# Kernel optimization log

Hardware: AMD Instinct MI355X
Metric: run time of the kernel (lower is better)

Reference implementation:

```python
import jax, jax.numpy as jnp
import numpy as np

NUM_BINS_X = 128; NUM_BINS_Y = 128
XL, XH, YL, YH = 0.0, 1000.0, 0.0, 1000.0
NUM_NETS = 100000
NUM_NODES = 200000
NUM_MOVABLE = 180000
NUM_PINS = 400000
UNIT_H_CAP = 1.5
UNIT_V_CAP = 1.4
MAX_RATE = 2.0
MIN_RATE = 1.0 / MAX_RATE
BIN_SX = (XH - XL) / NUM_BINS_X
BIN_SY = (YH - YL) / NUM_BINS_Y


def setup_inputs() -> dict:
    key = jax.random.key(0)
    k1, k2, k3, k4, k5, k6, k7, k8 = jax.random.split(key, 8)
    pos = jnp.concatenate([
        jax.random.uniform(k1, (NUM_NODES,), jnp.float32, XL, XH - 8.0),
        jax.random.uniform(k2, (NUM_NODES,), jnp.float32, YL, YH - 8.0)])
    pin_pos = jnp.concatenate([
        jax.random.uniform(k3, (NUM_PINS,), jnp.float32, XL, XH),
        jax.random.uniform(k4, (NUM_PINS,), jnp.float32, YL, YH)])
    node_size_x = jax.random.uniform(k5, (NUM_NODES,), jnp.float32, 1.0, 8.0)
    node_size_y = jax.random.uniform(k6, (NUM_NODES,), jnp.float32, 1.0, 8.0)
    # 4 pins per net (uniform ragged layout); flat_netpin is a permutation of pins
    netpin_start = jnp.arange(NUM_NETS + 1, dtype=jnp.int32) * (NUM_PINS // NUM_NETS)
    flat_netpin = jax.random.permutation(k7, NUM_PINS).astype(jnp.int32)
    net_weights = jax.random.uniform(k8, (NUM_NETS,), jnp.float32, 0.5, 1.5)
    return dict(pos=pos, pin_pos=pin_pos, node_size_x=node_size_x,
                node_size_y=node_size_y, net_weights=net_weights,
                netpin_start=netpin_start, flat_netpin=flat_netpin)


def _bin_edges(lo, size, n):
    l = lo + jnp.arange(n, dtype=jnp.float32) * size
    return l, l + size


def _overlap(lo_e, hi_e, lo, hi):
    # per-interval overlap of [lo, hi] with each bin [lo_e, hi_e]; >=0
    return jnp.clip(jnp.minimum(hi_e[None, :], hi[:, None]) -
                    jnp.maximum(lo_e[None, :], lo[:, None]), 0.0, None)


def reference(pos, pin_pos, node_size_x, node_size_y, net_weights,
              netpin_start, flat_netpin):
    # ---- phase 1: per-net bbox (ragged gather) + RUDY demand binning ----
    lengths = netpin_start[1:] - netpin_start[:-1]                      # [N]
    net_ids = jnp.repeat(jnp.arange(NUM_NETS, dtype=jnp.int32), lengths,
                         total_repeat_length=NUM_PINS)                  # [P]
    px = pin_pos[flat_netpin]
    py = pin_pos[flat_netpin + NUM_PINS]
    x_min = jax.ops.segment_min(px, net_ids, num_segments=NUM_NETS)
    x_max = jax.ops.segment_max(px, net_ids, num_segments=NUM_NETS)
    y_min = jax.ops.segment_min(py, net_ids, num_segments=NUM_NETS)
    y_max = jax.ops.segment_max(py, net_ids, num_segments=NUM_NETS)

    bxl, bxr = _bin_edges(XL, BIN_SX, NUM_BINS_X)
    byl, byr = _bin_edges(YL, BIN_SY, NUM_BINS_Y)
    ox = _overlap(bxl, bxr, x_min, x_max)                               # [N, BX]
    oy = _overlap(byl, byr, y_min, y_max)                               # [N, BY]
    dx = x_max - x_min
    dy = y_max - y_min
    # horizontal demand per bin = wt * overlap / (y_max - y_min); vertical analog
    cx = jnp.where(dy > 0, net_weights / jnp.where(dy > 0, dy, 1.0), 0.0)
    cy = jnp.where(dx > 0, net_weights / jnp.where(dx > 0, dx, 1.0), 0.0)
    map_x = jnp.einsum('nx,ny->xy', ox * cx[:, None], oy)               # [BX, BY]
    map_y = jnp.einsum('nx,ny->xy', ox * cy[:, None], oy)

    bin_area = BIN_SX * BIN_SY
    ux = map_x / (bin_area * UNIT_H_CAP)
    uy = map_y / (bin_area * UNIT_V_CAP)
    util = jnp.clip(jnp.maximum(ux, uy), MIN_RATE, MAX_RATE)            # [BX, BY]

    # ---- phase 2: per movable node, overlap-weighted utilization read-back ----
    nx = pos[:NUM_MOVABLE]
    ny = pos[NUM_NODES:NUM_NODES + NUM_MOVABLE]
    sx = node_size_x[:NUM_MOVABLE]
    sy = node_size_y[:NUM_MOVABLE]
    oxn = _overlap(bxl, bxr, nx, nx + sx)                               # [M, BX]
    oyn = _overlap(byl, byr, ny, ny + sy)                               # [M, BY]
    tmp = jnp.einsum('mx,xy->my', oxn, util)                            # [M, BY]
    instance_route_area = jnp.sum(tmp * oyn, axis=1)                    # [M]
    return instance_route_area
```

## Files before the change

### kernel.cpp

```cpp
#include <hip/hip_runtime.h>

constexpr int   NB         = 128;
constexpr int   NCELL      = NB * NB;
constexpr float S          = 7.8125f;
constexpr int   NUM_NETS   = 100000;
constexpr int   NUM_NODES  = 200000;
constexpr int   NUM_MOVABLE= 180000;
constexpr int   NUM_PINS   = 400000;
constexpr float UNIT_H_CAP = 1.5f;
constexpr float UNIT_V_CAP = 1.4f;

#define TPB    512
#define NDB    256
#define NCHUNK 4

__device__ __forceinline__ float edgef(int t) { return (float)t * S; }

__device__ __forceinline__ int bin_of(float v) {
    int t = (int)floorf(v / S);
    while (edgef(t + 1) <= v) ++t;
    while (edgef(t)     >  v) --t;
    return t;
}

__device__ __forceinline__ float phi(int t, float lo, float hi) {
    return fminf(fmaxf(edgef(t), lo), hi);
}

__device__ __forceinline__ int second_diff(float lo, float hi,
                                           int* idx, float* val) {
    int a = bin_of(lo);
    int b = bin_of(hi);
    int n = 0;
    idx[n] = a;
    val[n] = phi(a + 1, lo, hi) - 2.f * phi(a, lo, hi) + phi(a - 1, lo, hi);
    ++n;
    idx[n] = a + 1;
    val[n] = phi(a + 2, lo, hi) - 2.f * phi(a + 1, lo, hi) + phi(a, lo, hi);
    ++n;
    if (b > a + 1) {
        idx[n] = b;
        val[n] = phi(b + 1, lo, hi) - 2.f * phi(b, lo, hi) + phi(b - 1, lo, hi);
        ++n;
    }
    if (b > a) {
        idx[n] = b + 1;
        val[n] = phi(b + 2, lo, hi) - 2.f * phi(b + 1, lo, hi) + phi(b, lo, hi);
        ++n;
    }
    return n;
}

__global__ __launch_bounds__(TPB) void net_diff_kernel(
    const float* __restrict__ pin_pos,
    const float* __restrict__ net_weights,
    const int*   __restrict__ nps,
    const int*   __restrict__ fnp,
    float* __restrict__ Px, float* __restrict__ Py) {
    __shared__ float D[NCELL];
    const int tid = threadIdx.x;
    const int n   = blockIdx.x * TPB + tid;
    const bool have = (n < NUM_NETS);

    float4* D4 = (float4*)D;
    for (int i = tid; i < NCELL / 4; i += TPB) D4[i] = make_float4(0,0,0,0);

    float cx = 0.f, cy = 0.f;
    int ixs[4], iys[4];
    float vxs[4], vys[4];
    int nx = 0, ny = 0;

    if (have) {
        int s = nps[n], e = nps[n + 1];
        float xmin = 1e30f, xmax = -1e30f, ymin = 1e30f, ymax = -1e30f;
        if (e - s == 4 && (s & 3) == 0) {
            int4 p4 = *(const int4*)(fnp + s);
            float x0 = pin_pos[p4.x], y0 = pin_pos[p4.x + NUM_PINS];
            float x1 = pin_pos[p4.y], y1 = pin_pos[p4.y + NUM_PINS];
            float x2 = pin_pos[p4.z], y2 = pin_pos[p4.z + NUM_PINS];
            float x3 = pin_pos[p4.w], y3 = pin_pos[p4.w + NUM_PINS];
            xmin = fminf(fminf(x0, x1), fminf(x2, x3));
            xmax = fmaxf(fmaxf(x0, x1), fmaxf(x2, x3));
            ymin = fminf(fminf(y0, y1), fminf(y2, y3));
            ymax = fmaxf(fmaxf(y0, y1), fmaxf(y2, y3));
        } else {
            for (int p = s; p < e; ++p) {
                int pin = fnp[p];
                float px = pin_pos[pin];
                float py = pin_pos[pin + NUM_PINS];
                xmin = fminf(xmin, px); xmax = fmaxf(xmax, px);
                ymin = fminf(ymin, py); ymax = fmaxf(ymax, py);
            }
        }
        if (e > s) {
            float w  = net_weights[n];
            float dx = xmax - xmin, dy = ymax - ymin;
            cx = (dy > 0.f) ? w / dy : 0.f;
            cy = (dx > 0.f) ? w / dx : 0.f;
            if (cx != 0.f || cy != 0.f) {
                nx = second_diff(xmin, xmax, ixs, vxs);
                ny = second_diff(ymin, ymax, iys, vys);
            }
        }
    }
    __syncthreads();

    if (have && cx != 0.f) {
        for (int i = 0; i < nx; ++i) {
            int row = ixs[i];
            float cfi = cx * vxs[i];
            if (cfi == 0.f || row >= NB) continue;
            for (int j = 0; j < ny; ++j) {
                int col = iys[j];
                float t = cfi * vys[j];
                if (t == 0.f || col >= NB) continue;
                atomicAdd(&D[row * NB + col], t);
            }
        }
    }
    __syncthreads();
    {
        float4* P = (float4*)(Px + (size_t)blockIdx.x * NCELL);
        for (int i = tid; i < NCELL / 4; i += TPB) {
            P[i] = D4[i];
            D4[i] = make_float4(0,0,0,0);
        }
    }
    __syncthreads();

    if (have && cy != 0.f) {
        for (int i = 0; i < nx; ++i) {
            int row = ixs[i];
            float cfi = cy * vxs[i];
            if (cfi == 0.f || row >= NB) continue;
            for (int j = 0; j < ny; ++j) {
                int col = iys[j];
                float t = cfi * vys[j];
                if (t == 0.f || col >= NB) continue;
                atomicAdd(&D[row * NB + col], t);
            }
        }
    }
    __syncthreads();
    {
        float4* P = (float4*)(Py + (size_t)blockIdx.x * NCELL);
        for (int i = tid; i < NCELL / 4; i += TPB) P[i] = D4[i];
    }
}

__global__ __launch_bounds__(256) void reduce_kernel(
    const float4* __restrict__ Px, const float4* __restrict__ Py,
    float4* __restrict__ R, int B) {
    constexpr int NC4 = NCELL / 4;
    int t = blockIdx.x * blockDim.x + threadIdx.x;
    int chunk = blockIdx.y;
    if (t >= 2 * NC4) return;
    int m  = (t < NC4) ? 0 : 1;
    int c4 = t & (NC4 - 1);
    const float4* P = m ? Py : Px;
    int per = (B + NCHUNK - 1) / NCHUNK;
    int b0 = chunk * per;
    int b1 = min(b0 + per, B);
    float4 a0 = {0,0,0,0}, a1 = {0,0,0,0};
    int b = b0;
    for (; b + 1 < b1; b += 2) {
        float4 v0 = P[(size_t)b * NC4 + c4];
        float4 v1 = P[(size_t)(b + 1) * NC4 + c4];
        a0.x += v0.x; a0.y += v0.y; a0.z += v0.z; a0.w += v0.w;
        a1.x += v1.x; a1.y += v1.y; a1.z += v1.z; a1.w += v1.w;
    }
    for (; b < b1; ++b) {
        float4 v = P[(size_t)b * NC4 + c4];
        a0.x += v.x; a0.y += v.y; a0.z += v.z; a0.w += v.w;
    }
    float4 r;
    r.x = a0.x + a1.x; r.y = a0.y + a1.y; r.z = a0.z + a1.z; r.w = a0.w + a1.w;
    R[((size_t)(chunk * 2 + m)) * NC4 + c4] = r;
}

__global__ __launch_bounds__(256) void finish_kernel(
    const float* __restrict__ R,
    float* __restrict__ Xp,
    float* __restrict__ util) {
    int t = threadIdx.x;
    int m   = (t >= NB) ? 1 : 0;
    int col = t & (NB - 1);
    const float* Ra = R + (size_t)m * NCELL;
    float* O = Xp + (size_t)m * NCELL;
    float acc = 0.f;
    #pragma unroll 8
    for (int i = 0; i < NB; ++i) {
        int idx = i * NB + col;
        float v = Ra[idx] + Ra[2 * NCELL + idx] + Ra[4 * NCELL + idx]
                + Ra[6 * NCELL + idx];
        acc += v;
        O[idx] = acc;
    }
    __syncthreads();
    if (t < NB) {
        constexpr float invx = 1.f / (S * S * UNIT_H_CAP);
        constexpr float invy = 1.f / (S * S * UNIT_V_CAP);
        const float* Xx = Xp;
        const float* Xy = Xp + NCELL;
        float ax = 0.f, ay = 0.f;
        #pragma unroll 8
        for (int j = 0; j < NB; ++j) {
            int idx = t * NB + j;
            ax += Xx[idx];
            ay += Xy[idx];
            float u = fmaxf(ax * invx, ay * invy);
            util[idx] = fminf(fmaxf(u, 0.5f), 2.0f);
        }
    }
}

__global__ __launch_bounds__(256) void node_kernel(
    const float* __restrict__ pos,
    const float* __restrict__ nsx,
    const float* __restrict__ nsy,
    const float* __restrict__ util,
    float* __restrict__ out) {
    int m = blockIdx.x * blockDim.x + threadIdx.x;
    if (m >= NUM_MOVABLE) return;
    float x  = pos[m];
    float y  = pos[NUM_NODES + m];
    float xh = x + nsx[m];
    float yh = y + nsy[m];
    int ax = max(0,      (int)floorf(x  / S) - 1);
    int bx = min(NB - 1, (int)floorf(xh / S) + 1);
    int ay = max(0,      (int)floorf(y  / S) - 1);
    int by = min(NB - 1, (int)floorf(yh / S) + 1);
    float acc = 0.f;
    for (int i = ax; i <= bx; ++i) {
        float ov = fminf(edgef(i + 1), xh) - fmaxf(edgef(i), x);
        if (ov <= 0.f) continue;
        float inner = 0.f;
        for (int j = ay; j <= by; ++j) {
            float ovy = fminf(edgef(j + 1), yh) - fmaxf(edgef(j), y);
            if (ovy > 0.f) inner += ovy * util[i * NB + j];
        }
        acc += ov * inner;
    }
    out[m] = acc;
}

extern "C" void kernel_launch(void* const* d_in, const int* in_sizes, int n_in,
                              void* d_out, int out_size, void* d_ws, size_t ws_size,
                              hipStream_t stream) {
    const float* pos      = (const float*)d_in[0];
    const float* pin_pos  = (const float*)d_in[1];
    const float* nsx      = (const float*)d_in[2];
    const float* nsy      = (const float*)d_in[3];
    const float* nw       = (const float*)d_in[4];
    const int*   npstart  = (const int*)d_in[5];
    const int*   fnp      = (const int*)d_in[6];
    float*       out      = (float*)d_out;

    float* w    = (float*)d_ws;
    float* R    = w;                       w += NCHUNK * 2 * NCELL;
    float* Xp   = w;                       w += 2 * NCELL;
    float* util = w;                       w += NCELL;
    float* Px   = w;

    size_t fixed = (size_t)(w - (float*)d_ws) * sizeof(float);
    int B = NDB;
    if (ws_size > fixed) {
        size_t fit = (ws_size - fixed) / ((size_t)2 * NCELL * sizeof(float));
        if ((size_t)B > fit) B = (int)fit;
    } else {
        B = 1;
    }
    if (B < 1) B = 1;
    float* Py = Px + (size_t)B * NCELL;

    net_diff_kernel<<<B, TPB, 0, stream>>>(pin_pos, nw, npstart, fnp, Px, Py);
    {
        dim3 g((2 * (NCELL / 4) + 255) / 256, NCHUNK);
        reduce_kernel<<<g, 256, 0, stream>>>(
            (const float4*)Px, (const float4*)Py, (float4*)R, B);
    }
    finish_kernel<<<1, 256, 0, stream>>>(R, Xp, util);
    node_kernel<<<(NUM_MOVABLE + 255) / 256, 256, 0, stream>>>(
        pos, nsx, nsy, util, out);
}
```

Baseline: 133.1 us.

## Interleave partial-sum reduction across 8 slices and prefetch pin loads before smem clear

The reduce kernel now splits the per-block partial maps into 8 interleaved slices (block index strided by NPAR) instead of 4 contiguous chunks, and uses 4 accumulators per thread for more memory-level parallelism. The finish kernel sums 8 partials instead of 4. In the net kernel, pin-position and weight gathers are issued before the shared-memory zeroing loop so their latency overlaps the clear. The risks are more partial-result traffic and more serial summation work in the single-block finish kernel, and the launch hardcodes 256 reduce blocks, which assumes 2*NC4/256 = 32 slices times 8.

New measurement: 142.1 us. 6.8% more time.

```diff
diff --git a/kernel.cpp b/kernel.cpp
--- a/kernel.cpp
+++ b/kernel.cpp
@@ -12,7 +12,7 @@
 
 #define TPB    512
 #define NDB    256
-#define NCHUNK 4
+#define NPAR   8
 
 __device__ __forceinline__ float edgef(int t) { return (float)t * S; }
 
@@ -62,6 +62,22 @@
     const int n   = blockIdx.x * TPB + tid;
     const bool have = (n < NUM_NETS);
 
+    float x0=0,x1=0,x2=0,x3=0,y0=0,y1=0,y2=0,y3=0,w=0;
+    int s = 0, e = 0;
+    bool fast = false;
+    if (have) {
+        s = nps[n]; e = nps[n + 1];
+        fast = (e - s == 4) && ((s & 3) == 0);
+        if (fast) {
+            int4 p4 = *(const int4*)(fnp + s);
+            x0 = pin_pos[p4.x]; y0 = pin_pos[p4.x + NUM_PINS];
+            x1 = pin_pos[p4.y]; y1 = pin_pos[p4.y + NUM_PINS];
+            x2 = pin_pos[p4.z]; y2 = pin_pos[p4.z + NUM_PINS];
+            x3 = pin_pos[p4.w]; y3 = pin_pos[p4.w + NUM_PINS];
+            w  = net_weights[n];
+        }
+    }
+
     float4* D4 = (float4*)D;
     for (int i = tid; i < NCELL / 4; i += TPB) D4[i] = make_float4(0,0,0,0);
 
@@ -71,19 +87,14 @@
     int nx = 0, ny = 0;
 
     if (have) {
-        int s = nps[n], e = nps[n + 1];
-        float xmin = 1e30f, xmax = -1e30f, ymin = 1e30f, ymax = -1e30f;
-        if (e - s == 4 && (s & 3) == 0) {
-            int4 p4 = *(const int4*)(fnp + s);
-            float x0 = pin_pos[p4.x], y0 = pin_pos[p4.x + NUM_PINS];
-            float x1 = pin_pos[p4.y], y1 = pin_pos[p4.y + NUM_PINS];
-            float x2 = pin_pos[p4.z], y2 = pin_pos[p4.z + NUM_PINS];
-            float x3 = pin_pos[p4.w], y3 = pin_pos[p4.w + NUM_PINS];
+        float xmin, xmax, ymin, ymax;
+        if (fast) {
             xmin = fminf(fminf(x0, x1), fminf(x2, x3));
             xmax = fmaxf(fmaxf(x0, x1), fmaxf(x2, x3));
             ymin = fminf(fminf(y0, y1), fminf(y2, y3));
             ymax = fmaxf(fmaxf(y0, y1), fmaxf(y2, y3));
         } else {
+            xmin = 1e30f; xmax = -1e30f; ymin = 1e30f; ymax = -1e30f;
             for (int p = s; p < e; ++p) {
                 int pin = fnp[p];
                 float px = pin_pos[pin];
@@ -91,9 +102,9 @@
                 xmin = fminf(xmin, px); xmax = fmaxf(xmax, px);
                 ymin = fminf(ymin, py); ymax = fmaxf(ymax, py);
             }
+            if (e > s) w = net_weights[n];
         }
         if (e > s) {
-            float w  = net_weights[n];
             float dx = xmax - xmin, dy = ymax - ymin;
             cx = (dy > 0.f) ? w / dy : 0.f;
             cy = (dx > 0.f) ? w / dx : 0.f;
@@ -152,30 +163,35 @@
     const float4* __restrict__ Px, const float4* __restrict__ Py,
     float4* __restrict__ R, int B) {
     constexpr int NC4 = NCELL / 4;
-    int t = blockIdx.x * blockDim.x + threadIdx.x;
-    int chunk = blockIdx.y;
-    if (t >= 2 * NC4) return;
-    int m  = (t < NC4) ? 0 : 1;
-    int c4 = t & (NC4 - 1);
+    int L = blockIdx.x;
+    int p = L & (NPAR - 1);
+    int sl = L >> 3;
+    int g = sl * 256 + threadIdx.x;
+    int m  = (g < NC4) ? 0 : 1;
+    int c4 = g & (NC4 - 1);
     const float4* P = m ? Py : Px;
-    int per = (B + NCHUNK - 1) / NCHUNK;
-    int b0 = chunk * per;
-    int b1 = min(b0 + per, B);
-    float4 a0 = {0,0,0,0}, a1 = {0,0,0,0};
-    int b = b0;
-    for (; b + 1 < b1; b += 2) {
+    float4 a0 = {0,0,0,0}, a1 = {0,0,0,0}, a2 = {0,0,0,0}, a3 = {0,0,0,0};
+    int b = p;
+    for (; b + 3 * NPAR < B; b += 4 * NPAR) {
         float4 v0 = P[(size_t)b * NC4 + c4];
-        float4 v1 = P[(size_t)(b + 1) * NC4 + c4];
+        float4 v1 = P[(size_t)(b + NPAR) * NC4 + c4];
+        float4 v2 = P[(size_t)(b + 2 * NPAR) * NC4 + c4];
+        float4 v3 = P[(size_t)(b + 3 * NPAR) * NC4 + c4];
         a0.x += v0.x; a0.y += v0.y; a0.z += v0.z; a0.w += v0.w;
         a1.x += v1.x; a1.y += v1.y; a1.z += v1.z; a1.w += v1.w;
-    }
-    for (; b < b1; ++b) {
+        a2.x += v2.x; a2.y += v2.y; a2.z += v2.z; a2.w += v2.w;
+        a3.x += v3.x; a3.y += v3.y; a3.z += v3.z; a3.w += v3.w;
+    }
+    for (; b < B; b += NPAR) {
         float4 v = P[(size_t)b * NC4 + c4];
         a0.x += v.x; a0.y += v.y; a0.z += v.z; a0.w += v.w;
     }
     float4 r;
-    r.x = a0.x + a1.x; r.y = a0.y + a1.y; r.z = a0.z + a1.z; r.w = a0.w + a1.w;
-    R[((size_t)(chunk * 2 + m)) * NC4 + c4] = r;
+    r.x = (a0.x + a1.x) + (a2.x + a3.x);
+    r.y = (a0.y + a1.y) + (a2.y + a3.y);
+    r.z = (a0.z + a1.z) + (a2.z + a3.z);
+    r.w = (a0.w + a1.w) + (a2.w + a3.w);
+    R[(size_t)p * (2 * NC4) + g] = r;
 }
 
 __global__ __launch_bounds__(256) void finish_kernel(
@@ -188,11 +204,13 @@
     const float* Ra = R + (size_t)m * NCELL;
     float* O = Xp + (size_t)m * NCELL;
     float acc = 0.f;
-    #pragma unroll 8
+    #pragma unroll 4
     for (int i = 0; i < NB; ++i) {
         int idx = i * NB + col;
-        float v = Ra[idx] + Ra[2 * NCELL + idx] + Ra[4 * NCELL + idx]
-                + Ra[6 * NCELL + idx];
+        float v = 0.f;
+        #pragma unroll
+        for (int p = 0; p < NPAR; ++p)
+            v += Ra[(size_t)p * (2 * NCELL) + idx];
         acc += v;
         O[idx] = acc;
     }
@@ -257,7 +275,7 @@
     float*       out      = (float*)d_out;
 
     float* w    = (float*)d_ws;
-    float* R    = w;                       w += NCHUNK * 2 * NCELL;
+    float* R    = w;                       w += NPAR * 2 * NCELL;
     float* Xp   = w;                       w += 2 * NCELL;
     float* util = w;                       w += NCELL;
     float* Px   = w;
@@ -274,11 +292,8 @@
     float* Py = Px + (size_t)B * NCELL;
 
     net_diff_kernel<<<B, TPB, 0, stream>>>(pin_pos, nw, npstart, fnp, Px, Py);
-    {
-        dim3 g((2 * (NCELL / 4) + 255) / 256, NCHUNK);
-        reduce_kernel<<<g, 256, 0, stream>>>(
-            (const float4*)Px, (const float4*)Py, (float4*)R, B);
-    }
+    reduce_kernel<<<NDB, 256, 0, stream>>>(
+        (const float4*)Px, (const float4*)Py, (float4*)R, B);
     finish_kernel<<<1, 256, 0, stream>>>(R, Xp, util);
     node_kernel<<<(NUM_MOVABLE + 255) / 256, 256, 0, stream>>>(
         pos, nsx, nsy, util, out);
```
